# Kernel optimization log

Measured on AMD Instinct MI355X. Metric: run time of the kernel, lower is better.

## Reference

```python
import jax, jax.numpy as jnp
import numpy as np

B, S, D = 4, 2048, 1024
LN_EPS = 1e-3  # keras LayerNormalization default epsilon


def setup_inputs() -> dict:
    key = jax.random.key(0)
    ks = jax.random.split(key, 6)
    context = jax.random.normal(ks[0], (B, S, D), jnp.float32)
    eos_mask = jax.random.randint(ks[1], (B, 1, S, S), 0, 2).astype(jnp.int32)
    prior = jax.random.uniform(ks[2], (1,), jnp.float32)
    ln_gamma = jnp.ones((D,), jnp.float32)
    ln_beta = jnp.zeros((D,), jnp.float32)
    Wk = jax.random.normal(ks[3], (D, D), jnp.float32) / np.float32(np.sqrt(D))
    bk = jnp.zeros((D,), jnp.float32)
    Wq = jax.random.normal(ks[4], (D, D), jnp.float32) / np.float32(np.sqrt(D))
    bq = jnp.zeros((D,), jnp.float32)
    return dict(context=context, eos_mask=eos_mask, prior=prior,
                ln_gamma=ln_gamma, ln_beta=ln_beta, Wk=Wk, bk=bk, Wq=Wq, bq=bq)


def reference(context, eos_mask, prior, ln_gamma, ln_beta, Wk, bk, Wq, bq):
    seq_len = context.shape[1]
    d_model = jnp.float32(context.shape[-1])
    eos = jnp.squeeze(eos_mask, 1)  # [B,S,S]

    # LayerNorm over last axis
    mu = jnp.mean(context, axis=-1, keepdims=True)
    var = jnp.var(context, axis=-1, keepdims=True)
    x = (context - mu) * jax.lax.rsqrt(var + LN_EPS) * ln_gamma + ln_beta

    # constant band / triangular matrices
    a_mat = jnp.eye(seq_len, k=1, dtype=jnp.float32)
    b_mat = jnp.eye(seq_len, dtype=jnp.float32)
    c_mat = jnp.eye(seq_len, k=-1, dtype=jnp.float32)
    tri = jnp.triu(jnp.ones((seq_len, seq_len), jnp.float32))

    # mask: eos AND (super- or sub-diagonal)
    mask = ((eos != 0) & ((a_mat + c_mat) == 1.0)).astype(jnp.float32)

    k = x @ Wk + bk  # [B,S,D]
    q = x @ Wq + bq  # [B,S,D]
    scores = jnp.einsum('bqd,bkd->bqk', q, k) / d_model + mask * 1e-19
    neibor_attn = jax.nn.softmax(scores, axis=-1)
    neibor_attn = jnp.sqrt(jnp.square(neibor_attn + 1e-9))
    neibor_attn = prior + (1.0 - prior) * neibor_attn  # prior [1] broadcasts

    # log-domain cumulative (triangular) matmuls
    t_mat = jnp.einsum('bij,jk->bik', jnp.log(neibor_attn + 1e-9) * a_mat, tri)
    g_attn = jnp.exp(jnp.einsum('ij,bjk->bik', tri, t_mat)) * (tri - b_mat)
    g_attn = g_attn + jnp.transpose(g_attn, (0, 2, 1)) + (neibor_attn * b_mat + 1e-9)
    return (g_attn, neibor_attn)
```

## Files before the change

kernel.cpp:

```cpp
#include <hip/hip_runtime.h>

#define S_LEN 2048
#define D_MODEL 1024
#define NB 4

typedef unsigned short u16;
typedef __attribute__((ext_vector_type(8))) short short8;
typedef __attribute__((ext_vector_type(4))) float f32x4;
typedef __attribute__((ext_vector_type(4))) unsigned short u16x4;

__device__ inline u16 f2bf(float f) {
  union { float f; unsigned u; } v; v.f = f;
  unsigned u = v.u;
  unsigned r = (u + 0x7FFFu + ((u >> 16) & 1u)) >> 16;
  return (u16)r;
}

__device__ inline float bf2f(u16 b) {
  union { unsigned u; float f; } v; v.u = ((unsigned)b) << 16;
  return v.f;
}

__device__ inline void glds16(const void* g, void* l) {
  __builtin_amdgcn_global_load_lds((const __attribute__((address_space(1))) void*)g,
                                   (__attribute__((address_space(3))) void*)l,
                                   16, 0, 0);
}

__global__ __launch_bounds__(256) void w2_kernel(const float* __restrict__ Wk,
                                                 const float* __restrict__ bq,
                                                 float* __restrict__ w2) {
  const int r = blockIdx.x * 4 + (threadIdx.x >> 6);
  const int lane = threadIdx.x & 63;
  const f32x4* row = (const f32x4*)(Wk + (size_t)r * D_MODEL);
  float s = 0.0f;
  #pragma unroll
  for (int c = 0; c < 4; ++c) {
    const f32x4 v = row[lane * 4 + c];
    const f32x4 b = ((const f32x4*)bq)[lane * 4 + c];
    s += v[0]*b[0] + v[1]*b[1] + v[2]*b[2] + v[3]*b[3];
  }
  for (int o = 32; o > 0; o >>= 1) s += __shfl_xor(s, o);
  if (lane == 0) w2[r] = s;
}

__global__ __launch_bounds__(256) void ln_kernel(const float* __restrict__ ctx,
                                                 const float* __restrict__ gamma,
                                                 const float* __restrict__ beta,
                                                 const float* __restrict__ w2,
                                                 u16* __restrict__ xb,
                                                 float* __restrict__ bvec) {
  const int row = blockIdx.x;
  const int t = threadIdx.x;
  const f32x4 v = ((const f32x4*)(ctx + (size_t)row * D_MODEL))[t];
  float s = v[0] + v[1] + v[2] + v[3];
  float q = v[0]*v[0] + v[1]*v[1] + v[2]*v[2] + v[3]*v[3];
  for (int o = 32; o > 0; o >>= 1) { s += __shfl_xor(s, o); q += __shfl_xor(q, o); }
  __shared__ float rs[4], rq[4], rd[4];
  const int wave = t >> 6, lane = t & 63;
  if (lane == 0) { rs[wave] = s; rq[wave] = q; }
  __syncthreads();
  s = rs[0] + rs[1] + rs[2] + rs[3];
  q = rq[0] + rq[1] + rq[2] + rq[3];
  const float mu = s * (1.0f / D_MODEL);
  const float var = q * (1.0f / D_MODEL) - mu * mu;
  const float rstd = rsqrtf(var + 1e-3f);
  const f32x4 g4 = ((const f32x4*)gamma)[t];
  const f32x4 b4 = ((const f32x4*)beta)[t];
  const f32x4 w4 = ((const f32x4*)w2)[t];
  float xv[4];
  float dot = 0.0f;
  #pragma unroll
  for (int u = 0; u < 4; ++u) {
    xv[u] = (v[u] - mu) * rstd * g4[u] + b4[u];
    dot += xv[u] * w4[u];
  }
  u16x4 o;
  #pragma unroll
  for (int u = 0; u < 4; ++u) o[u] = f2bf(xv[u]);
  ((u16x4*)(xb + (size_t)row * D_MODEL))[t] = o;
  for (int of = 32; of > 0; of >>= 1) dot += __shfl_xor(dot, of);
  if (lane == 0) rd[wave] = dot;
  __syncthreads();
  if (t == 0) bvec[row] = (rd[0] + rd[1] + rd[2] + rd[3]) * (1.0f / D_MODEL);
}

__global__ __launch_bounds__(256) void prep_w(const float* __restrict__ Wq,
                                              const float* __restrict__ Wk,
                                              u16* __restrict__ Wt) {
  __shared__ float tile[32][33];
  const int k0 = blockIdx.x * 32;
  const int n0 = blockIdx.y * 32;
  const int tx = threadIdx.x, ty = threadIdx.y;
  const float* W = (n0 < D_MODEL) ? Wq : Wk;
  const int nl0 = (n0 < D_MODEL) ? n0 : (n0 - D_MODEL);
  #pragma unroll
  for (int j = 0; j < 32; j += 8)
    tile[ty + j][tx] = W[(size_t)(k0 + ty + j) * D_MODEL + nl0 + tx];
  __syncthreads();
  #pragma unroll
  for (int j = 0; j < 32; j += 8)
    Wt[(size_t)(n0 + ty + j) * D_MODEL + k0 + tx] = f2bf(tile[tx][ty + j]);
}

__global__ __launch_bounds__(256, 2) void gemm_bt(
    const u16* __restrict__ A, int lda, long long sA,
    const u16* __restrict__ Bt, int ldb, long long sB,
    u16* __restrict__ C, int ldc, long long sC,
    float scale, int K) {
  __shared__ u16 As[128][32];
  __shared__ u16 Bs[128][32];
  const int tid = threadIdx.x;
  const int wave = tid >> 6, lane = tid & 63;
  const int z = blockIdx.z;
  A += (size_t)z * sA;
  Bt += (size_t)z * sB;
  const size_t m0 = (size_t)blockIdx.y * 128;
  const size_t n0 = (size_t)blockIdx.x * 128;
  const int wr = (wave >> 1) * 64;
  const int wc = (wave & 1) * 64;
  const int strow = wave * 16 + (lane >> 2);
  const int stslot = (lane & 3) * 8;
  const int fr = lane & 15, fq = lane >> 4;

  f32x4 acc[4][4];
  #pragma unroll
  for (int i = 0; i < 4; ++i)
    #pragma unroll
    for (int j = 0; j < 4; ++j) acc[i][j] = (f32x4)(0.0f);

  for (int k0 = 0; k0 < K; k0 += 32) {
    const u16* ga = A + (m0 + strow) * lda + k0 + stslot;
    const u16* gb = Bt + (n0 + strow) * ldb + k0 + stslot;
    glds16(ga, &As[wave * 16][0]);
    glds16(ga + (size_t)64 * lda, &As[64 + wave * 16][0]);
    glds16(gb, &Bs[wave * 16][0]);
    glds16(gb + (size_t)64 * ldb, &Bs[64 + wave * 16][0]);
    __syncthreads();
    short8 af[4], bfv[4];
    #pragma unroll
    for (int mi = 0; mi < 4; ++mi) af[mi] = *(const short8*)&As[wr + mi * 16 + fr][fq * 8];
    #pragma unroll
    for (int ni = 0; ni < 4; ++ni) bfv[ni] = *(const short8*)&Bs[wc + ni * 16 + fr][fq * 8];
    #pragma unroll
    for (int mi = 0; mi < 4; ++mi)
      #pragma unroll
      for (int ni = 0; ni < 4; ++ni)
        acc[mi][ni] = __builtin_amdgcn_mfma_f32_16x16x32_bf16(af[mi], bfv[ni], acc[mi][ni], 0, 0, 0);
    __syncthreads();
  }

  #pragma unroll
  for (int mi = 0; mi < 4; ++mi)
    #pragma unroll
    for (int ni = 0; ni < 4; ++ni) {
      const size_t row = m0 + wr + mi * 16 + fq * 4;
      const size_t col = n0 + wc + ni * 16 + fr;
      #pragma unroll
      for (int r = 0; r < 4; ++r)
        C[((size_t)z * sC) + (row + r) * ldc + col] = f2bf(acc[mi][ni][r] * scale);
    }
}

__global__ __launch_bounds__(512, 2) void gemm8p256(
    const u16* __restrict__ A, int lda, long long sA,
    const u16* __restrict__ Bt, int ldb, long long sB,
    u16* __restrict__ C, int ldc, long long sC,
    float scale, int K) {
  __shared__ char smem[131072];
  const int tid = threadIdx.x;
  const int wave = tid >> 6, lane = tid & 63;
  const int fr = lane & 15, fq = lane >> 4;
  const int wm = wave >> 2, wn = wave & 3;
  const int z = blockIdx.z;
  const size_t m0 = (size_t)blockIdx.y * 256;
  const size_t n0 = (size_t)blockIdx.x * 256;
  const u16* Ab = A + (size_t)z * sA + m0 * lda;
  const u16* Bb = Bt + (size_t)z * sB + n0 * ldb;
  const int perA = (lane >> 3) * lda + (((lane & 7) ^ (lane >> 3)) * 8);
  const int perB = (lane >> 3) * ldb + (((lane & 7) ^ (lane >> 3)) * 8);
  const int u0v = wave * 2, u1v = wave * 2 + 1;
  const int rA_0 = (u0v & 7) * 8 + (u0v >> 3) * 128;
  const int rA_1 = (u1v & 7) * 8 + (u1v >> 3) * 128;
  const int rB_0 = (u0v >> 2) * 64 + (u0v & 3) * 8;
  const int rB_1 = (u1v >> 2) * 64 + (u1v & 3) * 8;
  const int sw0 = ((fq) ^ (fr & 7)) * 16;
  const int sw1 = ((4 + fq) ^ (fr & 7)) * 16;
  const int aBase = wm * 16384 + fr * 128;
  const int bBase = 32768 + wn * 8192 + fr * 128;

  f32x4 acc[8][4];
  #pragma unroll
  for (int i = 0; i < 8; ++i)
    #pragma unroll
    for (int j = 0; j < 4; ++j) acc[i][j] = (f32x4)(0.0f);

#define STG_A02(BUF, KK) do { \
    glds16(Ab + (size_t)rA_0 * lda + perA + (KK), smem + (BUF) + rA_0 * 128); \
    glds16(Ab + (size_t)rA_1 * lda + perA + (KK), smem + (BUF) + rA_1 * 128); } while (0)
#define STG_A13(BUF, KK) do { \
    glds16(Ab + (size_t)(rA_0 + 64) * lda + perA + (KK), smem + (BUF) + (rA_0 + 64) * 128); \
    glds16(Ab + (size_t)(rA_1 + 64) * lda + perA + (KK), smem + (BUF) + (rA_1 + 64) * 128); } while (0)
#define STG_BEV(BUF, KK) do { \
    glds16(Bb + (size_t)rB_0 * ldb + perB + (KK), smem + (BUF) + 32768 + rB_0 * 128); \
    glds16(Bb + (size_t)rB_1 * ldb + perB + (KK), smem + (BUF) + 32768 + rB_1 * 128); } while (0)
#define STG_BOD(BUF, KK) do { \
    glds16(Bb + (size_t)(rB_0 + 32) * ldb + perB + (KK), smem + (BUF) + 32768 + (rB_0 + 32) * 128); \
    glds16(Bb + (size_t)(rB_1 + 32) * ldb + perB + (KK), smem + (BUF) + 32768 + (rB_1 + 32) * 128); } while (0)

  const int NT = K >> 6;
  STG_A02(0, 0); STG_BEV(0, 0); STG_BOD(0, 0); STG_A13(0, 0);

  for (int t = 0; t < NT; ++t) {
    const int bo = (t & 1) * 65536;
    const int bn = bo ^ 65536;
    const int kk = (t + 1 < NT) ? (t + 1) * 64 : 0;
    short8 a0[8], a1[8], be[4], bod[4];

    asm volatile("s_waitcnt vmcnt(4)" ::: "memory");
    asm volatile("s_barrier" ::: "memory");
    #pragma unroll
    for (int fi = 0; fi < 4; ++fi) {
      a0[fi * 2 + 0] = *(const short8*)(smem + bo + aBase + fi * 2048 + sw0);
      a0[fi * 2 + 1] = *(const short8*)(smem + bo + aBase + fi * 2048 + sw1);
    }
    #pragma unroll
    for (int nj = 0; nj < 2; ++nj) {
      be[nj * 2 + 0] = *(const short8*)(smem + bo + bBase + nj * 2048 + sw0);
      be[nj * 2 + 1] = *(const short8*)(smem + bo + bBase + nj * 2048 + sw1);
    }
    STG_A02(bn, kk);
    __builtin_amdgcn_s_setprio(1);
    #pragma unroll
    for (int ks = 0; ks < 2; ++ks)
      #pragma unroll
      for (int fi = 0; fi < 4; ++fi)
        #pragma unroll
        for (int nj = 0; nj < 2; ++nj)
          acc[fi][nj] = __builtin_amdgcn_mfma_f32_16x16x32_bf16(a0[fi * 2 + ks], be[nj * 2 + ks], acc[fi][nj], 0, 0, 0);
    __builtin_amdgcn_s_setprio(0);

    asm volatile("s_waitcnt vmcnt(4)" ::: "memory");
    asm volatile("s_barrier" ::: "memory");
    #pragma unroll
    for (int nj = 0; nj < 2; ++nj) {
      bod[nj * 2 + 0] = *(const short8*)(smem + bo + bBase + 4096 + nj * 2048 + sw0);
      bod[nj * 2 + 1] = *(const short8*)(smem + bo + bBase + 4096 + nj * 2048 + sw1);
    }
    STG_BEV(bn, kk);
    __builtin_amdgcn_s_setprio(1);
    #pragma unroll
    for (int ks = 0; ks < 2; ++ks)
      #pragma unroll
      for (int fi = 0; fi < 4; ++fi)
        #pragma unroll
        for (int nj = 0; nj < 2; ++nj)
          acc[fi][2 + nj] = __builtin_amdgcn_mfma_f32_16x16x32_bf16(a0[fi * 2 + ks], bod[nj * 2 + ks], acc[fi][2 + nj], 0, 0, 0);
    __builtin_amdgcn_s_setprio(0);

    asm volatile("s_waitcnt vmcnt(4)" ::: "memory");
    asm volatile("s_barrier" ::: "memory");
    #pragma unroll
    for (int fi = 0; fi < 4; ++fi) {
      a1[fi * 2 + 0] = *(const short8*)(smem + bo + aBase + 8192 + fi * 2048 + sw0);
      a1[fi * 2 + 1] = *(const short8*)(smem + bo + aBase + 8192 + fi * 2048 + sw1);
    }
    STG_BOD(bn, kk);
    __builtin_amdgcn_s_setprio(1);
    #pragma unroll
    for (int ks = 0; ks < 2; ++ks)
      #pragma unroll
      for (int fi = 0; fi < 4; ++fi)
        #pragma unroll
        for (int nj = 0; nj < 2; ++nj)
          acc[4 + fi][nj] = __builtin_amdgcn_mfma_f32_16x16x32_bf16(a1[fi * 2 + ks], be[nj * 2 + ks], acc[4 + fi][nj], 0, 0, 0);
    __builtin_amdgcn_s_setprio(0);

    asm volatile("s_barrier" ::: "memory");
    STG_A13(bn, kk);
    __builtin_amdgcn_s_setprio(1);
    #pragma unroll
    for (int ks = 0; ks < 2; ++ks)
      #pragma unroll
      for (int fi = 0; fi < 4; ++fi)
        #pragma unroll
        for (int nj = 0; nj < 2; ++nj)
          acc[4 + fi][2 + nj] = __builtin_amdgcn_mfma_f32_16x16x32_bf16(a1[fi * 2 + ks], bod[nj * 2 + ks], acc[4 + fi][2 + nj], 0, 0, 0);
    __builtin_amdgcn_s_setprio(0);
  }
#undef STG_A02
#undef STG_A13
#undef STG_BEV
#undef STG_BOD

  u16* Cz = C + (size_t)z * sC;
  #pragma unroll
  for (int mi = 0; mi < 8; ++mi)
    #pragma unroll
    for (int ni = 0; ni < 4; ++ni) {
      const size_t row = m0 + wm * 128 + (mi >> 2) * 64 + (mi & 3) * 16 + fq * 4;
      const size_t col = n0 + wn * 64 + (ni >> 1) * 32 + (ni & 1) * 16 + fr;
      #pragma unroll
      for (int r = 0; r < 4; ++r)
        Cz[(row + r) * ldc + col] = f2bf(acc[mi][ni][r] * scale);
    }
}

__global__ __launch_bounds__(512, 2) void gemm8p128(
    const u16* __restrict__ A, int lda, long long sA,
    const u16* __restrict__ Bt, int ldb, long long sB,
    u16* __restrict__ C, int ldc, long long sC,
    float scale, int K) {
  __shared__ char smem[98304];
  const int tid = threadIdx.x;
  const int wave = tid >> 6, lane = tid & 63;
  const int fr = lane & 15, fq = lane >> 4;
  const int wm = wave >> 2, wn = wave & 3;
  const int z = blockIdx.z;
  const size_t m0 = (size_t)blockIdx.y * 128;
  const size_t n0 = (size_t)blockIdx.x * 256;
  const u16* Ab = A + (size_t)z * sA + m0 * lda;
  const u16* Bb = Bt + (size_t)z * sB + n0 * ldb;
  const int perA = (lane >> 3) * lda + (((lane & 7) ^ (lane >> 3)) * 8);
  const int perB = (lane >> 3) * ldb + (((lane & 7) ^ (lane >> 3)) * 8);
  const int u0v = wave * 2, u1v = wave * 2 + 1;
  const int rA_0 = u0v * 8;
  const int rA_1 = u1v * 8;
  const int rB_0 = (u0v >> 2) * 64 + (u0v & 3) * 8;
  const int rB_1 = (u1v >> 2) * 64 + (u1v & 3) * 8;
  const int sw0 = ((fq) ^ (fr & 7)) * 16;
  const int sw1 = ((4 + fq) ^ (fr & 7)) * 16;
  const int aBase = wm * 8192 + fr * 128;
  const int bBase = 16384 + wn * 8192 + fr * 128;

  f32x4 acc[4][4];
  #pragma unroll
  for (int i = 0; i < 4; ++i)
    #pragma unroll
    for (int j = 0; j < 4; ++j) acc[i][j] = (f32x4)(0.0f);

#define STG_A(BUF, KK) do { \
    glds16(Ab + (size_t)rA_0 * lda + perA + (KK), smem + (BUF) + rA_0 * 128); \
    glds16(Ab + (size_t)rA_1 * lda + perA + (KK), smem + (BUF) + rA_1 * 128); } while (0)
#define STG_BEV(BUF, KK) do { \
    glds16(Bb + (size_t)rB_0 * ldb + perB + (KK), smem + (BUF) + 16384 + rB_0 * 128); \
    glds16(Bb + (size_t)rB_1 * ldb + perB + (KK), smem + (BUF) + 16384 + rB_1 * 128); } while (0)
#define STG_BOD(BUF, KK) do { \
    glds16(Bb + (size_t)(rB_0 + 32) * ldb + perB + (KK), smem + (BUF) + 16384 + (rB_0 + 32) * 128); \
    glds16(Bb + (size_t)(rB_1 + 32) * ldb + perB + (KK), smem + (BUF) + 16384 + (rB_1 + 32) * 128); } while (0)

  const int NT = K >> 6;
  STG_A(0, 0); STG_BEV(0, 0); STG_BOD(0, 0);

  for (int t = 0; t < NT; ++t) {
    const int bo = (t & 1) * 49152;
    const int bn = bo ^ 49152;
    const int kk = (t + 1 < NT) ? (t + 1) * 64 : 0;
    short8 af[8], bv[4];

    asm volatile("s_waitcnt vmcnt(2)" ::: "memory");
    asm volatile("s_barrier" ::: "memory");
    #pragma unroll
    for (int fi = 0; fi < 4; ++fi) {
      af[fi * 2 + 0] = *(const short8*)(smem + bo + aBase + fi * 2048 + sw0);
      af[fi * 2 + 1] = *(const short8*)(smem + bo + aBase + fi * 2048 + sw1);
    }
    #pragma unroll
    for (int nj = 0; nj < 2; ++nj) {
      bv[nj * 2 + 0] = *(const short8*)(smem + bo + bBase + nj * 2048 + sw0);
      bv[nj * 2 + 1] = *(const short8*)(smem + bo + bBase + nj * 2048 + sw1);
    }
    STG_A(bn, kk);
    STG_BEV(bn, kk);
    __builtin_amdgcn_s_setprio(1);
    #pragma unroll
    for (int ks = 0; ks < 2; ++ks)
      #pragma unroll
      for (int fi = 0; fi < 4; ++fi)
        #pragma unroll
        for (int nj = 0; nj < 2; ++nj)
          acc[fi][nj] = __builtin_amdgcn_mfma_f32_16x16x32_bf16(af[fi * 2 + ks], bv[nj * 2 + ks], acc[fi][nj], 0, 0, 0);
    __builtin_amdgcn_s_setprio(0);

    asm volatile("s_waitcnt vmcnt(4)" ::: "memory");
    asm volatile("s_barrier" ::: "memory");
    #pragma unroll
    for (int nj = 0; nj < 2; ++nj) {
      bv[nj * 2 + 0] = *(const short8*)(smem + bo + bBase + 4096 + nj * 2048 + sw0);
      bv[nj * 2 + 1] = *(const short8*)(smem + bo + bBase + 4096 + nj * 2048 + sw1);
    }
    STG_BOD(bn, kk);
    __builtin_amdgcn_s_setprio(1);
    #pragma unroll
    for (int ks = 0; ks < 2; ++ks)
      #pragma unroll
      for (int fi = 0; fi < 4; ++fi)
        #pragma unroll
        for (int nj = 0; nj < 2; ++nj)
          acc[fi][2 + nj] = __builtin_amdgcn_mfma_f32_16x16x32_bf16(af[fi * 2 + ks], bv[nj * 2 + ks], acc[fi][2 + nj], 0, 0, 0);
    __builtin_amdgcn_s_setprio(0);
  }
#undef STG_A
#undef STG_BEV
#undef STG_BOD

  u16* Cz = C + (size_t)z * sC;
  #pragma unroll
  for (int fi = 0; fi < 4; ++fi)
    #pragma unroll
    for (int ni = 0; ni < 4; ++ni) {
      const size_t row = m0 + wm * 64 + fi * 16 + fq * 4;
      const size_t col = n0 + wn * 64 + (ni >> 1) * 32 + (ni & 1) * 16 + fr;
      #pragma unroll
      for (int r = 0; r < 4; ++r)
        Cz[(row + r) * ldc + col] = f2bf(acc[fi][ni][r] * scale);
    }
}

__global__ __launch_bounds__(256) void softmax_kernel(const u16* __restrict__ Sb,
                                                      const float* __restrict__ bvec,
                                                      const float* __restrict__ prior,
                                                      float* __restrict__ na,
                                                      float* __restrict__ ell,
                                                      float* __restrict__ dvec) {
  const int row = blockIdx.x;
  const int t = threadIdx.x;
  const int b = row >> 11, i = row & (S_LEN - 1);
  const short8 sv = ((const short8*)(Sb + (size_t)row * S_LEN))[t];
  const f32x4 bv0 = ((const f32x4*)(bvec + (size_t)b * S_LEN))[t * 2];
  const f32x4 bv1 = ((const f32x4*)(bvec + (size_t)b * S_LEN))[t * 2 + 1];
  float v[8];
  #pragma unroll
  for (int u = 0; u < 8; ++u)
    v[u] = bf2f((u16)sv[u]) + ((u < 4) ? bv0[u] : bv1[u - 4]);
  float mx = v[0];
  #pragma unroll
  for (int u = 1; u < 8; ++u) mx = fmaxf(mx, v[u]);
  for (int o = 32; o > 0; o >>= 1) mx = fmaxf(mx, __shfl_xor(mx, o));
  __shared__ float red[4], red2[4];
  const int wave = t >> 6, lane = t & 63;
  if (lane == 0) red[wave] = mx;
  __syncthreads();
  mx = fmaxf(fmaxf(red[0], red[1]), fmaxf(red[2], red[3]));
  float e[8], s = 0.0f;
  #pragma unroll
  for (int u = 0; u < 8; ++u) { e[u] = __expf(v[u] - mx); s += e[u]; }
  for (int o = 32; o > 0; o >>= 1) s += __shfl_xor(s, o);
  if (lane == 0) red2[wave] = s;
  __syncthreads();
  s = red2[0] + red2[1] + red2[2] + red2[3];
  const float pr = prior[0];
  const float w = 1.0f - pr;
  const float inv = 1.0f / s;
  f32x4 o0, o1;
  #pragma unroll
  for (int u = 0; u < 4; ++u) o0[u] = pr + w * (e[u] * inv + 1e-9f);
  #pragma unroll
  for (int u = 0; u < 4; ++u) o1[u] = pr + w * (e[4 + u] * inv + 1e-9f);
  f32x4* nrow = (f32x4*)(na + (size_t)row * S_LEN);
  nrow[t * 2] = o0;
  nrow[t * 2 + 1] = o1;
  #pragma unroll
  for (int u = 0; u < 8; ++u) {
    const int j = t * 8 + u;
    const float ov = (u < 4) ? o0[u] : o1[u - 4];
    if (j == i) dvec[row] = ov;
    if (j == i + 1) ell[row] = logf(ov + 1e-9f);
  }
  if (i == S_LEN - 1 && t == 0) ell[row] = 0.0f;
}

__global__ __launch_bounds__(256) void scan_kernel(const float* __restrict__ ell,
                                                   float* __restrict__ Cpre) {
  const int b = blockIdx.x, t = threadIdx.x;
  const float* eb = ell + (size_t)b * S_LEN;
  const f32x4 e0 = ((const f32x4*)eb)[t * 2];
  const f32x4 e1 = ((const f32x4*)eb)[t * 2 + 1];
  float ev[8];
  #pragma unroll
  for (int u = 0; u < 4; ++u) ev[u] = e0[u];
  #pragma unroll
  for (int u = 0; u < 4; ++u) ev[4 + u] = e1[u];
  float loc[8], tot = 0.0f;
  #pragma unroll
  for (int u = 0; u < 8; ++u) { loc[u] = tot; tot += ev[u]; }
  __shared__ float sbuf[256];
  sbuf[t] = tot;
  __syncthreads();
  for (int off = 1; off < 256; off <<= 1) {
    const float v = (t >= off) ? sbuf[t - off] : 0.0f;
    __syncthreads();
    sbuf[t] += v;
    __syncthreads();
  }
  const float base = (t == 0) ? 0.0f : sbuf[t - 1];
  #pragma unroll
  for (int u = 0; u < 8; ++u)
    Cpre[(size_t)b * S_LEN + t * 8 + u] = base + loc[u];
}

__global__ __launch_bounds__(256) void gattn_kernel(const float* __restrict__ Cpre,
                                                    const float* __restrict__ dvec,
                                                    float* __restrict__ g) {
  const int b = blockIdx.z, i = blockIdx.y;
  const int j0 = blockIdx.x * 1024 + threadIdx.x * 4;
  const float Ci = Cpre[b * S_LEN + i];
  const float di = dvec[b * S_LEN + i];
  const f32x4 Cj = *(const f32x4*)&Cpre[b * S_LEN + j0];
  f32x4 o;
  #pragma unroll
  for (int u = 0; u < 4; ++u) {
    const int j = j0 + u;
    const float arg = (j > i) ? (Cj[u] - Ci) : (Ci - Cj[u]);
    o[u] = (j == i) ? (di + 1e-9f) : (__expf(arg) + 1e-9f);
  }
  *(f32x4*)(g + ((size_t)b * S_LEN + i) * S_LEN + j0) = o;
}

extern "C" void kernel_launch(void* const* d_in, const int* in_sizes, int n_in,
                              void* d_out, int out_size, void* d_ws, size_t ws_size,
                              hipStream_t stream) {
  const float* ctx   = (const float*)d_in[0];
  const float* prior = (const float*)d_in[2];
  const float* gamma = (const float*)d_in[3];
  const float* beta  = (const float*)d_in[4];
  const float* Wk    = (const float*)d_in[5];
  const float* Wq    = (const float*)d_in[7];
  const float* bq    = (const float*)d_in[8];

  float* g  = (float*)d_out;
  float* na = g + (size_t)NB * S_LEN * S_LEN;

  u16* Xb = (u16*)na;
  u16* Yb = Xb + (size_t)(NB * S_LEN) * D_MODEL;
  u16* PT = Yb + (size_t)(NB * S_LEN) * D_MODEL;
  u16* Wt = PT + (size_t)D_MODEL * D_MODEL;
  u16* Sb = (u16*)g;
  float* w2   = (float*)d_ws;
  float* bvec = w2 + D_MODEL;
  float* ell  = bvec + NB * S_LEN;
  float* dvec = ell + NB * S_LEN;
  float* Cpre = dvec + NB * S_LEN;

  w2_kernel<<<D_MODEL / 4, 256, 0, stream>>>(Wk, bq, w2);
  ln_kernel<<<NB * S_LEN, 256, 0, stream>>>(ctx, gamma, beta, w2, Xb, bvec);
  prep_w<<<dim3(32, 64), dim3(32, 8), 0, stream>>>(Wq, Wk, Wt);

  gemm_bt<<<dim3(8, 8, 1), 256, 0, stream>>>(Wt + (size_t)D_MODEL * D_MODEL, D_MODEL, 0,
                                             Wt, D_MODEL, 0,
                                             PT, D_MODEL, 0, 1.0f, D_MODEL);
  gemm8p128<<<dim3(4, 64, 1), 512, 0, stream>>>(Xb, D_MODEL, 0,
                                                PT, D_MODEL, 0,
                                                Yb, D_MODEL, 0, 1.0f, D_MODEL);
  gemm8p256<<<dim3(8, 8, NB), 512, 0, stream>>>(Yb, D_MODEL, (long long)S_LEN * D_MODEL,
                                                Xb, D_MODEL, (long long)S_LEN * D_MODEL,
                                                Sb, S_LEN, (long long)S_LEN * S_LEN,
                                                1.0f / (float)D_MODEL, D_MODEL);

  softmax_kernel<<<NB * S_LEN, 256, 0, stream>>>(Sb, bvec, prior, na, ell, dvec);
  scan_kernel<<<NB, 256, 0, stream>>>(ell, Cpre);
  gattn_kernel<<<dim3(2, S_LEN, NB), 256, 0, stream>>>(Cpre, dvec, g);
}
```

Measured before the change: 136.1 us.

## Deepen GEMM prefetch pipelines and remap blocks across XCDs

Both bf16 GEMM kernels now remap the linear block index so that consecutive tiles land on the same XCD, which should improve L2 reuse. The 256x256 kernel rotates its staging order so the A02 quarter of the tile after next is prefetched into the freed buffer. The 128x256 kernel moves from double to triple buffering in 144 KB of LDS and waits on deeper vmcnt thresholds. The aim is to hide more global-load latency behind MFMA work, at the cost of more LDS use per block and possibly lower occupancy.

```diff
diff --git a/kernel.cpp b/kernel.cpp
--- a/kernel.cpp
+++ b/kernel.cpp
@@ -25,6 +25,18 @@
   __builtin_amdgcn_global_load_lds((const __attribute__((address_space(1))) void*)g,
                                    (__attribute__((address_space(3))) void*)l,
                                    16, 0, 0);
+}
+
+__device__ inline void xcd_remap(int& bx, int& by, int& bz) {
+  const int gx = gridDim.x, gy = gridDim.y;
+  const int gxy = gx * gy;
+  const int total = gxy * (int)gridDim.z;
+  int lin = ((int)blockIdx.z * gy + (int)blockIdx.y) * gx + (int)blockIdx.x;
+  lin = (lin & 7) * (total >> 3) + (lin >> 3);
+  bz = lin / gxy;
+  int rem = lin - bz * gxy;
+  by = rem / gx;
+  bx = rem - by * gx;
 }
 
 __global__ __launch_bounds__(256) void w2_kernel(const float* __restrict__ Wk,
@@ -172,9 +184,11 @@
   const int wave = tid >> 6, lane = tid & 63;
   const int fr = lane & 15, fq = lane >> 4;
   const int wm = wave >> 2, wn = wave & 3;
-  const int z = blockIdx.z;
-  const size_t m0 = (size_t)blockIdx.y * 256;
-  const size_t n0 = (size_t)blockIdx.x * 256;
+  int bx, by, bz;
+  xcd_remap(bx, by, bz);
+  const int z = bz;
+  const size_t m0 = (size_t)by * 256;
+  const size_t n0 = (size_t)bx * 256;
   const u16* Ab = A + (size_t)z * sA + m0 * lda;
   const u16* Bb = Bt + (size_t)z * sB + n0 * ldb;
   const int perA = (lane >> 3) * lda + (((lane & 7) ^ (lane >> 3)) * 8);
@@ -210,14 +224,16 @@
 
   const int NT = K >> 6;
   STG_A02(0, 0); STG_BEV(0, 0); STG_BOD(0, 0); STG_A13(0, 0);
+  STG_A02(65536, (NT > 1) ? 64 : 0);
 
   for (int t = 0; t < NT; ++t) {
     const int bo = (t & 1) * 65536;
     const int bn = bo ^ 65536;
-    const int kk = (t + 1 < NT) ? (t + 1) * 64 : 0;
+    const int kk  = (t + 1 < NT) ? (t + 1) * 64 : 0;
+    const int kk2 = (t + 2 < NT) ? (t + 2) * 64 : 0;
     short8 a0[8], a1[8], be[4], bod[4];
 
-    asm volatile("s_waitcnt vmcnt(4)" ::: "memory");
+    asm volatile("s_waitcnt vmcnt(6)" ::: "memory");
     asm volatile("s_barrier" ::: "memory");
     #pragma unroll
     for (int fi = 0; fi < 4; ++fi) {
@@ -229,7 +245,7 @@
       be[nj * 2 + 0] = *(const short8*)(smem + bo + bBase + nj * 2048 + sw0);
       be[nj * 2 + 1] = *(const short8*)(smem + bo + bBase + nj * 2048 + sw1);
     }
-    STG_A02(bn, kk);
+    STG_BEV(bn, kk);
     __builtin_amdgcn_s_setprio(1);
     #pragma unroll
     for (int ks = 0; ks < 2; ++ks)
@@ -240,14 +256,14 @@
           acc[fi][nj] = __builtin_amdgcn_mfma_f32_16x16x32_bf16(a0[fi * 2 + ks], be[nj * 2 + ks], acc[fi][nj], 0, 0, 0);
     __builtin_amdgcn_s_setprio(0);
 
-    asm volatile("s_waitcnt vmcnt(4)" ::: "memory");
+    asm volatile("s_waitcnt vmcnt(6)" ::: "memory");
     asm volatile("s_barrier" ::: "memory");
     #pragma unroll
     for (int nj = 0; nj < 2; ++nj) {
       bod[nj * 2 + 0] = *(const short8*)(smem + bo + bBase + 4096 + nj * 2048 + sw0);
       bod[nj * 2 + 1] = *(const short8*)(smem + bo + bBase + 4096 + nj * 2048 + sw1);
     }
-    STG_BEV(bn, kk);
+    STG_BOD(bn, kk);
     __builtin_amdgcn_s_setprio(1);
     #pragma unroll
     for (int ks = 0; ks < 2; ++ks)
@@ -258,14 +274,14 @@
           acc[fi][2 + nj] = __builtin_amdgcn_mfma_f32_16x16x32_bf16(a0[fi * 2 + ks], bod[nj * 2 + ks], acc[fi][2 + nj], 0, 0, 0);
     __builtin_amdgcn_s_setprio(0);
 
-    asm volatile("s_waitcnt vmcnt(4)" ::: "memory");
+    asm volatile("s_waitcnt vmcnt(6)" ::: "memory");
     asm volatile("s_barrier" ::: "memory");
     #pragma unroll
     for (int fi = 0; fi < 4; ++fi) {
       a1[fi * 2 + 0] = *(const short8*)(smem + bo + aBase + 8192 + fi * 2048 + sw0);
       a1[fi * 2 + 1] = *(const short8*)(smem + bo + aBase + 8192 + fi * 2048 + sw1);
     }
-    STG_BOD(bn, kk);
+    STG_A13(bn, kk);
     __builtin_amdgcn_s_setprio(1);
     #pragma unroll
     for (int ks = 0; ks < 2; ++ks)
@@ -277,7 +293,7 @@
     __builtin_amdgcn_s_setprio(0);
 
     asm volatile("s_barrier" ::: "memory");
-    STG_A13(bn, kk);
+    STG_A02(bo, kk2);
     __builtin_amdgcn_s_setprio(1);
     #pragma unroll
     for (int ks = 0; ks < 2; ++ks)
@@ -311,14 +327,16 @@
     const u16* __restrict__ Bt, int ldb, long long sB,
     u16* __restrict__ C, int ldc, long long sC,
     float scale, int K) {
-  __shared__ char smem[98304];
+  __shared__ char smem[147456];
   const int tid = threadIdx.x;
   const int wave = tid >> 6, lane = tid & 63;
   const int fr = lane & 15, fq = lane >> 4;
   const int wm = wave >> 2, wn = wave & 3;
-  const int z = blockIdx.z;
-  const size_t m0 = (size_t)blockIdx.y * 128;
-  const size_t n0 = (size_t)blockIdx.x * 256;
+  int bx, by, bz;
+  xcd_remap(bx, by, bz);
+  const int z = bz;
+  const size_t m0 = (size_t)by * 128;
+  const size_t n0 = (size_t)bx * 256;
   const u16* Ab = A + (size_t)z * sA + m0 * lda;
   const u16* Bb = Bt + (size_t)z * sB + n0 * ldb;
   const int perA = (lane >> 3) * lda + (((lane & 7) ^ (lane >> 3)) * 8);
@@ -351,14 +369,18 @@
 
   const int NT = K >> 6;
   STG_A(0, 0); STG_BEV(0, 0); STG_BOD(0, 0);
+  {
+    const int k1 = (NT > 1) ? 64 : 0;
+    STG_A(49152, k1); STG_BEV(49152, k1); STG_BOD(49152, k1);
+  }
 
   for (int t = 0; t < NT; ++t) {
-    const int bo = (t & 1) * 49152;
-    const int bn = bo ^ 49152;
-    const int kk = (t + 1 < NT) ? (t + 1) * 64 : 0;
+    const int bo = (t % 3) * 49152;
+    const int bs = ((t + 2) % 3) * 49152;
+    const int kk = (t + 2 < NT) ? (t + 2) * 64 : 0;
     short8 af[8], bv[4];
 
-    asm volatile("s_waitcnt vmcnt(2)" ::: "memory");
+    asm volatile("s_waitcnt vmcnt(8)" ::: "memory");
     asm volatile("s_barrier" ::: "memory");
     #pragma unroll
     for (int fi = 0; fi < 4; ++fi) {
@@ -370,8 +392,8 @@
       bv[nj * 2 + 0] = *(const short8*)(smem + bo + bBase + nj * 2048 + sw0);
       bv[nj * 2 + 1] = *(const short8*)(smem + bo + bBase + nj * 2048 + sw1);
     }
-    STG_A(bn, kk);
-    STG_BEV(bn, kk);
+    STG_A(bs, kk);
+    STG_BEV(bs, kk);
     __builtin_amdgcn_s_setprio(1);
     #pragma unroll
     for (int ks = 0; ks < 2; ++ks)
@@ -382,14 +404,14 @@
           acc[fi][nj] = __builtin_amdgcn_mfma_f32_16x16x32_bf16(af[fi * 2 + ks], bv[nj * 2 + ks], acc[fi][nj], 0, 0, 0);
     __builtin_amdgcn_s_setprio(0);
 
-    asm volatile("s_waitcnt vmcnt(4)" ::: "memory");
+    asm volatile("s_waitcnt vmcnt(10)" ::: "memory");
     asm volatile("s_barrier" ::: "memory");
     #pragma unroll
     for (int nj = 0; nj < 2; ++nj) {
       bv[nj * 2 + 0] = *(const short8*)(smem + bo + bBase + 4096 + nj * 2048 + sw0);
       bv[nj * 2 + 1] = *(const short8*)(smem + bo + bBase + 4096 + nj * 2048 + sw1);
     }
-    STG_BOD(bn, kk);
+    STG_BOD(bs, kk);
     __builtin_amdgcn_s_setprio(1);
     #pragma unroll
     for (int ks = 0; ks < 2; ++ks)
```

New measurement: 136.1 us. About the same (+0.1%).
